# Kernel tuning notes

Measured on AMD Instinct MI355X. Metric: run time of the kernel, lower is better.

The kernel has to match this reference:

```python
import jax, jax.numpy as jnp
import numpy as np

# DeepseekV2MOE config (DeepSeek-V2-Lite-like, scaled)
T, H, E, I, K = 1024, 1024, 64, 512, 6
G, TKG = 8, 3          # n_group, topk_group
N_SHARED = 2
C = 256
SCALE = 2.5            # routed_scaling_factor


def setup_inputs() -> dict:
    key = jax.random.key(0)
    ks = jax.random.split(key, 7)
    inv = lambda d: 1.0 / np.sqrt(d).astype(np.float32)
    return {
        "hidden_states": jax.random.normal(ks[0], (T, H), jnp.float32),
        "gate_w": jax.random.normal(ks[1], (H, E), jnp.float32) * inv(H),
        "e_bias": jax.random.normal(ks[2], (E,), jnp.float32) * 0.01,  # e_score_correction_bias (noaux_tc)
        "w_gate_up": jax.random.normal(ks[3], (E, H, 2 * I), jnp.float32) * inv(H),
        "w_down": jax.random.normal(ks[4], (E, I, H), jnp.float32) * inv(I),
        "ws_gate_up": jax.random.normal(ks[5], (H, 2 * I * N_SHARED), jnp.float32) * inv(H),
        "ws_down": jax.random.normal(ks[6], (I * N_SHARED, H), jnp.float32) * inv(I * N_SHARED),
    }


def _silu_and_mul(gu):
    g, u = jnp.split(gu, 2, axis=-1)
    return jax.nn.silu(g) * u


def _grouped_topk(logits, bias):
    # DeepSeek-V3 noaux_tc grouped top-k with sigmoid scoring.
    scores = jax.nn.sigmoid(logits)                              # [T,E] original scores
    s = scores + bias[None, :]                                   # bias-corrected scores for selection
    grp = s.reshape(-1, G, E // G)
    grp_score = jax.lax.top_k(grp, 2)[0].sum(-1)                 # [T,G] sum of top-2 per group
    gidx = jax.lax.top_k(grp_score, TKG)[1]                      # [T,TKG]
    t = jnp.arange(s.shape[0])[:, None]
    gmask = jnp.zeros_like(grp_score, dtype=bool).at[t, gidx].set(True)
    emask = jnp.repeat(gmask, E // G, axis=1)                    # [T,E]
    eidx = jax.lax.top_k(jnp.where(emask, s, -jnp.inf), K)[1]    # [T,K]
    w = jnp.take_along_axis(scores, eidx, axis=1)                # weights from original (un-biased) scores
    w = w / w.sum(-1, keepdims=True)                             # renormalize (norm_topk_prob)
    return w, eidx


def _fused_moe(x, w, eidx, w_gate_up, w_down):
    # capacity-based dispatch -> grouped GEMM -> gather/scale combine
    A = x.shape[0] * K
    ef = eidx.reshape(A)                                         # expert id per assignment
    oh = jax.nn.one_hot(ef, E, dtype=jnp.int32)                  # [A,E]
    pos = ((jnp.cumsum(oh, axis=0) - 1) * oh).sum(-1)            # slot of each assignment within its expert
    xr = jnp.repeat(x, K, axis=0)                                # [A,H]
    xe = jnp.zeros((E, C, x.shape[1]), x.dtype).at[ef, pos].set(xr, mode="drop")  # [E,C,H]
    act = _silu_and_mul(jnp.einsum("ech,ehf->ecf", xe, w_gate_up))                # [E,C,I]
    ye = jnp.einsum("eci,eih->ech", act, w_down)                                   # [E,C,H]
    keep = (pos < C).astype(x.dtype)[:, None]
    yf = ye[ef, jnp.minimum(pos, C - 1)] * keep                  # [A,H]
    return (yf.reshape(-1, K, x.shape[1]) * w[..., None]).sum(1)  # [T,H]


def reference(hidden_states, gate_w, e_bias, w_gate_up, w_down, ws_gate_up, ws_down):
    shared = _silu_and_mul(hidden_states @ ws_gate_up) @ ws_down   # shared experts MLP
    logits = hidden_states @ gate_w                                # router
    w, eidx = _grouped_topk(logits, e_bias)
    routed = _fused_moe(hidden_states, w, eidx, w_gate_up, w_down)
    return routed * SCALE + shared                                 # non-fp16 branch
```

## Files before the change

### kernel.cpp

```cpp
#include <hip/hip_runtime.h>
#include <math.h>

typedef __bf16 bf16;
typedef bf16 bf16x8 __attribute__((ext_vector_type(8)));
typedef float f32x4 __attribute__((ext_vector_type(4)));
typedef unsigned int u32;

#define T_DIM 1024
#define H_DIM 1024
#define E_NUM 64
#define I_DIM 512
#define KTOP 6
#define TKG 3
#define CAP 256
#define A_TOT (T_DIM * KTOP)
#define SCALE_F 2.5f

#define BMx 128
#define BNx 128
#define BKx 64

typedef const u32 __attribute__((address_space(1)))* gas_t;
typedef u32 __attribute__((address_space(3)))* las_t;
__device__ __forceinline__ void gld16(const void* g, void* l) {
  __builtin_amdgcn_global_load_lds((gas_t)(unsigned long long)g,
                                   (las_t)(u32)(unsigned long long)l, 16, 0, 0);
}

__global__ __launch_bounds__(256) void cvt_bf16(const float* __restrict__ in,
                                                bf16* __restrict__ out) {
  int i = (blockIdx.x * 256 + threadIdx.x) * 4;
  float4 v = *(const float4*)(in + i);
  bf16 __align__(8) t[4] = {(bf16)v.x, (bf16)v.y, (bf16)v.z, (bf16)v.w};
  *(uint2*)(out + i) = *(const uint2*)t;
}

__global__ __launch_bounds__(256) void transpose_cvt(const float* __restrict__ in,
                                                     bf16* __restrict__ out,
                                                     int R, int C) {
  __shared__ bf16 tile[64][68];
  const long bb = (long)blockIdx.z * R * C;
  in += bb;
  out += bb;
  const int r0 = blockIdx.x * 64, c0 = blockIdx.y * 64;
  const int tid = threadIdx.x;
  const int lr = tid >> 4;
  const int lc = (tid & 15) * 4;
  #pragma unroll
  for (int rr = 0; rr < 64; rr += 16) {
    float4 v = *(const float4*)(in + (long)(r0 + lr + rr) * C + c0 + lc);
    bf16 __align__(8) t4[4] = {(bf16)v.x, (bf16)v.y, (bf16)v.z, (bf16)v.w};
    *(uint2*)(&tile[lr + rr][lc]) = *(const uint2*)t4;
  }
  __syncthreads();
  const int orow = tid >> 3;
  const int oc = (tid & 7) * 8;
  #pragma unroll
  for (int p = 0; p < 64; p += 32) {
    bf16 __align__(16) t8[8];
    #pragma unroll
    for (int j = 0; j < 8; ++j) t8[j] = tile[oc + j][orow + p];
    *(uint4*)(out + (long)(c0 + orow + p) * R + r0 + oc) = *(const uint4*)t8;
  }
}

__global__ __launch_bounds__(256) void router_topk(const float* __restrict__ x,
                                                   const float* __restrict__ gw,
                                                   const float* __restrict__ bias,
                                                   int* __restrict__ topk_id,
                                                   float* __restrict__ topk_w) {
  __shared__ float part[4][64];
  const int t = blockIdx.x;
  const int tid = threadIdx.x;
  const int wave = tid >> 6, lane = tid & 63;
  const float* xr = x + (long)t * H_DIM + wave * 256;
  float acc = 0.f;
  for (int h = 0; h < 256; h += 4) {
    float4 xv = *(const float4*)(xr + h);
    int hh = wave * 256 + h;
    acc += xv.x * gw[(hh + 0) * E_NUM + lane];
    acc += xv.y * gw[(hh + 1) * E_NUM + lane];
    acc += xv.z * gw[(hh + 2) * E_NUM + lane];
    acc += xv.w * gw[(hh + 3) * E_NUM + lane];
  }
  part[wave][lane] = acc;
  __syncthreads();
  if (wave != 0) return;
  acc = part[0][lane] + part[1][lane] + part[2][lane] + part[3][lane];

  float score = 1.f / (1.f + __expf(-acc));
  float sel = score + bias[lane];

  float m1 = sel, m2 = -INFINITY;
  #pragma unroll
  for (int off = 1; off < 8; off <<= 1) {
    float o1 = __shfl_xor(m1, off);
    float o2 = __shfl_xor(m2, off);
    float mn = fminf(m1, o1);
    float alt = (m1 >= o1) ? m2 : o2;
    m1 = fmaxf(m1, o1);
    m2 = fmaxf(mn, alt);
  }
  float gscore = m1 + m2;

  const int my_g = lane >> 3;
  unsigned gmask = 0;
  float gv = ((lane & 7) == 0) ? gscore : -INFINITY;
  for (int r = 0; r < TKG; ++r) {
    float v = gv;
    int idx = my_g;
    #pragma unroll
    for (int off = 1; off < 64; off <<= 1) {
      float ov = __shfl_xor(v, off);
      int oi = __shfl_xor(idx, off);
      if (ov > v || (ov == v && oi < idx)) { v = ov; idx = oi; }
    }
    gmask |= 1u << idx;
    if (my_g == idx) gv = -INFINITY;
  }

  float cand = ((gmask >> my_g) & 1u) ? sel : -INFINITY;
  float wk[KTOP];
  int ik[KTOP];
  float wsum = 0.f;
  for (int r = 0; r < KTOP; ++r) {
    float v = cand;
    int idx = lane;
    #pragma unroll
    for (int off = 1; off < 64; off <<= 1) {
      float ov = __shfl_xor(v, off);
      int oi = __shfl_xor(idx, off);
      if (ov > v || (ov == v && oi < idx)) { v = ov; idx = oi; }
    }
    float w = __shfl(score, idx);
    wk[r] = w; ik[r] = idx; wsum += w;
    if (lane == idx) cand = -INFINITY;
  }
  if (lane == 0) {
    float inv = 1.f / wsum;
    #pragma unroll
    for (int r = 0; r < KTOP; ++r) {
      topk_id[t * KTOP + r] = ik[r];
      topk_w[t * KTOP + r] = wk[r] * inv;
    }
  }
}

__global__ __launch_bounds__(64) void dispatch(const int* __restrict__ topk_id,
                                               int* __restrict__ rowlist,
                                               int* __restrict__ slot_a,
                                               int* __restrict__ counts) {
  __shared__ int ids[A_TOT];
  const int e = blockIdx.x, lane = threadIdx.x;
  for (int i = lane; i < A_TOT; i += 64) ids[i] = topk_id[i];
  __syncthreads();
  int base = 0;
  for (int a0 = 0; a0 < A_TOT; a0 += 64) {
    int a = a0 + lane;
    bool m = (ids[a] == e);
    unsigned long long bal = __ballot(m);
    if (m) {
      int pos = base + __popcll(bal & ((1ull << lane) - 1ull));
      slot_a[a] = (pos < CAP) ? pos : -1;
      if (pos < CAP) rowlist[e * CAP + pos] = a;
    }
    base += __popcll(bal);
  }
  if (lane == 0) counts[e] = (base < CAP) ? base : CAP;
}


__global__ __launch_bounds__(256) void gemm_gu(
    const bf16* __restrict__ X, int x_ld,
    const int* __restrict__ rows, const int* __restrict__ counts, int n_rows_fixed,
    const bf16* __restrict__ BT, long b_estride, int u_off,
    bf16* __restrict__ act, int act_ld, long act_estride, int kdim) {
  __shared__ union {
    struct { bf16 A[BMx * BKx]; bf16 B[BNx * BKx]; } st;
    bf16 epi[BMx * 72];
  } sm;
  const int e = blockIdx.z;
  const int n_rows = counts ? counts[e] : n_rows_fixed;
  const int m0 = blockIdx.x * BMx;
  if (m0 >= n_rows) return;
  const int nb = blockIdx.y;
  const int tid = threadIdx.x;
  const int w = tid >> 6, lane = tid & 63;
  const int q = lane >> 4, l16 = lane & 15;
  const int m_off = (w & 1) * 64;

  const int srow = w * 32 + (lane >> 3);
  const int gchunk = (lane & 7) ^ (lane >> 3);
  const bf16* pA[4];
  const bf16* pB[4];
  #pragma unroll
  for (int j = 0; j < 4; ++j) {
    int tr = m0 + srow + j * 8;
    int grow;
    if (rows) grow = (tr < n_rows) ? (rows[e * CAP + tr] / KTOP) : 0;
    else grow = tr;
    pA[j] = X + (long)grow * x_ld + gchunk * 8;
    int rB = srow + j * 8;
    int ng = (rB < 64) ? (nb * 64 + rB) : (u_off + nb * 64 + (rB - 64));
    pB[j] = BT + (long)e * b_estride + (long)ng * kdim + gchunk * 8;
  }
  bf16* ldsA = sm.st.A + w * 2048 + lane * 8;
  bf16* ldsB = sm.st.B + w * 2048 + lane * 8;

  f32x4 acc[4][4];
  #pragma unroll
  for (int i = 0; i < 4; ++i)
    #pragma unroll
    for (int j = 0; j < 4; ++j) acc[i][j] = (f32x4){0.f, 0.f, 0.f, 0.f};

  for (int k0 = 0; k0 < kdim; k0 += BKx) {
    #pragma unroll
    for (int j = 0; j < 4; ++j) {
      gld16(pA[j], ldsA + j * 512);
      gld16(pB[j], ldsB + j * 512);
      pA[j] += BKx;
      pB[j] += BKx;
    }
    __syncthreads();
    #pragma unroll
    for (int kh = 0; kh < 2; ++kh) {
      const int co = ((kh * 4 + q) ^ (l16 & 7)) * 8;
      bf16x8 a[4], b[4];
      #pragma unroll
      for (int i = 0; i < 4; ++i)
        a[i] = *(const bf16x8*)(sm.st.A + (m_off + i * 16 + l16) * BKx + co);
      #pragma unroll
      for (int j = 0; j < 4; ++j) {
        int nf = (j >> 1) * 64 + (w >> 1) * 32 + (j & 1) * 16;
        b[j] = *(const bf16x8*)(sm.st.B + (nf + l16) * BKx + co);
      }
      #pragma unroll
      for (int i = 0; i < 4; ++i)
        #pragma unroll
        for (int j = 0; j < 4; ++j)
          acc[i][j] = __builtin_amdgcn_mfma_f32_16x16x32_bf16(a[i], b[j], acc[i][j], 0, 0, 0);
    }
    __syncthreads();
  }

  const int c_base = (w >> 1) * 32;
  #pragma unroll
  for (int i = 0; i < 4; ++i)
    #pragma unroll
    for (int j = 0; j < 2; ++j)
      #pragma unroll
      for (int r = 0; r < 4; ++r) {
        float g = acc[i][j][r], uu = acc[i][j + 2][r];
        float s = g / (1.f + __expf(-g));
        sm.epi[(m_off + i * 16 + q * 4 + r) * 72 + c_base + j * 16 + l16] = (bf16)(s * uu);
      }
  __syncthreads();
  #pragma unroll
  for (int p = 0; p < 4; ++p) {
    int row = p * 32 + (tid >> 3);
    int c0 = (tid & 7) * 8;
    uint4 v = *(const uint4*)(sm.epi + row * 72 + c0);
    *(uint4*)(act + (long)e * act_estride + (long)(m0 + row) * act_ld + nb * 64 + c0) = v;
  }
}

template <typename OutT>
__global__ __launch_bounds__(256) void gemm_dn(
    const bf16* __restrict__ Abase, long a_estride, int a_ld,
    const int* __restrict__ rowsO, const int* __restrict__ counts, int n_rows_fixed,
    const bf16* __restrict__ BT, long b_estride,
    OutT* __restrict__ Out, int out_ld, int kdim) {
  __shared__ union {
    struct { bf16 A[BMx * BKx]; bf16 B[BNx * BKx]; } st;
    bf16 epi[BMx * 136];
  } sm;
  const int e = blockIdx.z;
  const int n_rows = counts ? counts[e] : n_rows_fixed;
  const int m0 = blockIdx.x * BMx;
  if (m0 >= n_rows) return;
  const int nb = blockIdx.y;
  const int tid = threadIdx.x;
  const int w = tid >> 6, lane = tid & 63;
  const int q = lane >> 4, l16 = lane & 15;
  const int m_off = (w & 1) * 64;
  const int n_off = (w >> 1) * 64;

  const int srow = w * 32 + (lane >> 3);
  const int gchunk = (lane & 7) ^ (lane >> 3);
  const bf16* pA[4];
  const bf16* pB[4];
  #pragma unroll
  for (int j = 0; j < 4; ++j) {
    pA[j] = Abase + (long)e * a_estride + (long)(m0 + srow + j * 8) * a_ld + gchunk * 8;
    pB[j] = BT + (long)e * b_estride + (long)(nb * BNx + srow + j * 8) * kdim + gchunk * 8;
  }
  bf16* ldsA = sm.st.A + w * 2048 + lane * 8;
  bf16* ldsB = sm.st.B + w * 2048 + lane * 8;

  f32x4 acc[4][4];
  #pragma unroll
  for (int i = 0; i < 4; ++i)
    #pragma unroll
    for (int j = 0; j < 4; ++j) acc[i][j] = (f32x4){0.f, 0.f, 0.f, 0.f};

  for (int k0 = 0; k0 < kdim; k0 += BKx) {
    #pragma unroll
    for (int j = 0; j < 4; ++j) {
      gld16(pA[j], ldsA + j * 512);
      gld16(pB[j], ldsB + j * 512);
      pA[j] += BKx;
      pB[j] += BKx;
    }
    __syncthreads();
    #pragma unroll
    for (int kh = 0; kh < 2; ++kh) {
      const int co = ((kh * 4 + q) ^ (l16 & 7)) * 8;
      bf16x8 a[4], b[4];
      #pragma unroll
      for (int i = 0; i < 4; ++i)
        a[i] = *(const bf16x8*)(sm.st.A + (m_off + i * 16 + l16) * BKx + co);
      #pragma unroll
      for (int j = 0; j < 4; ++j)
        b[j] = *(const bf16x8*)(sm.st.B + (n_off + j * 16 + l16) * BKx + co);
      #pragma unroll
      for (int i = 0; i < 4; ++i)
        #pragma unroll
        for (int j = 0; j < 4; ++j)
          acc[i][j] = __builtin_amdgcn_mfma_f32_16x16x32_bf16(a[i], b[j], acc[i][j], 0, 0, 0);
    }
    __syncthreads();
  }

  if constexpr (sizeof(OutT) == 4) {
    #pragma unroll
    for (int i = 0; i < 4; ++i)
      #pragma unroll
      for (int j = 0; j < 4; ++j)
        #pragma unroll
        for (int r = 0; r < 4; ++r) {
          int row = m0 + m_off + i * 16 + q * 4 + r;
          Out[(long)row * out_ld + nb * BNx + n_off + j * 16 + l16] = acc[i][j][r];
        }
  } else {
    #pragma unroll
    for (int i = 0; i < 4; ++i)
      #pragma unroll
      for (int j = 0; j < 4; ++j)
        #pragma unroll
        for (int r = 0; r < 4; ++r)
          sm.epi[(m_off + i * 16 + q * 4 + r) * 136 + n_off + j * 16 + l16] = (bf16)acc[i][j][r];
    __syncthreads();
    #pragma unroll
    for (int p = 0; p < 8; ++p) {
      int row = p * 16 + (tid >> 4);
      int c0 = (tid & 15) * 8;
      if (m0 + row < n_rows) {
        long orow = rowsO ? (long)rowsO[e * CAP + m0 + row] : (long)(m0 + row);
        *(uint4*)((bf16*)Out + orow * out_ld + nb * BNx + c0) =
            *(const uint4*)(sm.epi + row * 136 + c0);
      }
    }
  }
}

__global__ __launch_bounds__(256) void combine(const float* __restrict__ tkw,
                                               const int* __restrict__ slot_a,
                                               const bf16* __restrict__ Ya,
                                               float* __restrict__ out) {
  const int t = blockIdx.x, tid = threadIdx.x;
  long o = (long)t * H_DIM + tid * 4;
  float4 v = *(float4*)(out + o);
  float a0 = v.x, a1 = v.y, a2 = v.z, a3 = v.w;
  #pragma unroll
  for (int k = 0; k < KTOP; ++k) {
    int a = t * KTOP + k;
    if (slot_a[a] >= 0) {
      float w = tkw[a] * SCALE_F;
      const bf16* yr = Ya + (long)a * H_DIM + tid * 4;
      uint2 yv = *(const uint2*)yr;
      bf16 __align__(8) yb[4];
      *(uint2*)yb = yv;
      a0 += w * (float)yb[0];
      a1 += w * (float)yb[1];
      a2 += w * (float)yb[2];
      a3 += w * (float)yb[3];
    }
  }
  *(float4*)(out + o) = make_float4(a0, a1, a2, a3);
}

extern "C" void kernel_launch(void* const* d_in, const int* in_sizes, int n_in,
                              void* d_out, int out_size, void* d_ws, size_t ws_size,
                              hipStream_t stream) {
  const float* x     = (const float*)d_in[0];
  const float* gw    = (const float*)d_in[1];
  const float* bias  = (const float*)d_in[2];
  const float* w_gu  = (const float*)d_in[3];
  const float* w_dn  = (const float*)d_in[4];
  const float* ws_gu = (const float*)d_in[5];
  const float* ws_dn = (const float*)d_in[6];
  float* out = (float*)d_out;
  char* ws = (char*)d_ws;

  bf16* xbf     = (bf16*)(ws + 0);
  bf16* acts    = (bf16*)(ws + 2097152);
  bf16* actr    = (bf16*)(ws + 4194304);
  bf16* Ya      = (bf16*)(ws + 20971520);
  int*  tki     = (int*)(ws + 33554432);
  float* tkw    = (float*)(ws + 33579008);
  int*  rowlist = (int*)(ws + 33603584);
  int*  slot_a  = (int*)(ws + 33669120);
  int*  counts  = (int*)(ws + 33693696);
  bf16* wsguT   = (bf16*)(ws + 33694720);
  bf16* wsdnT   = (bf16*)(ws + 37889024);
  bf16* wguT    = (bf16*)(ws + 39986176);
  bf16* wdnT    = (bf16*)(ws + 39986176);

  cvt_bf16<<<dim3((T_DIM * H_DIM) / 1024), dim3(256), 0, stream>>>(x, xbf);
  router_topk<<<dim3(T_DIM), dim3(256), 0, stream>>>(x, gw, bias, tki, tkw);
  dispatch<<<dim3(E_NUM), dim3(64), 0, stream>>>(tki, rowlist, slot_a, counts);

  transpose_cvt<<<dim3(16, 16, 64), dim3(256), 0, stream>>>(w_gu, wguT, H_DIM, 2 * I_DIM);
  transpose_cvt<<<dim3(16, 32, 1), dim3(256), 0, stream>>>(ws_gu, wsguT, H_DIM, 2048);
  transpose_cvt<<<dim3(16, 16, 1), dim3(256), 0, stream>>>(ws_dn, wsdnT, 1024, H_DIM);

  gemm_gu<<<dim3(CAP / BMx, I_DIM / 64, E_NUM), dim3(256), 0, stream>>>(
      xbf, H_DIM, rowlist, counts, 0,
      wguT, (long)(2 * I_DIM) * H_DIM, I_DIM,
      actr, I_DIM, (long)CAP * I_DIM, H_DIM);

  gemm_gu<<<dim3(T_DIM / BMx, 1024 / 64, 1), dim3(256), 0, stream>>>(
      xbf, H_DIM, nullptr, nullptr, T_DIM,
      wsguT, 0, 1024,
      acts, 1024, 0, H_DIM);

  transpose_cvt<<<dim3(8, 16, 64), dim3(256), 0, stream>>>(w_dn, wdnT, I_DIM, H_DIM);

  gemm_dn<bf16><<<dim3(CAP / BMx, H_DIM / BNx, E_NUM), dim3(256), 0, stream>>>(
      actr, (long)CAP * I_DIM, I_DIM, rowlist, counts, 0,
      wdnT, (long)H_DIM * I_DIM,
      (bf16*)Ya, H_DIM, I_DIM);

  gemm_dn<float><<<dim3(T_DIM / BMx, H_DIM / BNx, 1), dim3(256), 0, stream>>>(
      acts, 0, 1024, nullptr, nullptr, T_DIM,
      wsdnT, 0,
      out, H_DIM, 1024);

  combine<<<dim3(T_DIM), dim3(256), 0, stream>>>(tkw, slot_a, Ya, out);
}
```

Baseline: 662.0 us.

## Fuse fp32 weight transpose and bf16 conversion into GEMM B-tile loads

Removes the separate transpose_cvt passes over all expert and shared weights. The GEMM kernels now read fp32 weights directly in their original layout, convert them to bf16 in registers, and write transposed, swizzled tiles into LDS, with the next k-tile's loads prefetched into registers. This avoids writing a full bf16 copy of the weights and reading it back. In exchange it adds register pressure, conversion ALU work in the main loop, and makes the B loads synchronous register loads instead of direct-to-LDS loads.

New measurement: 595.9 us. -10.0%, faster.

```diff
diff --git a/kernel.cpp b/kernel.cpp
--- a/kernel.cpp
+++ b/kernel.cpp
@@ -27,41 +27,16 @@
                                    (las_t)(u32)(unsigned long long)l, 16, 0, 0);
 }
 
+__device__ __forceinline__ int bswz(int n) {
+  return ((n >> 2) ^ ((n & 3) << 1)) & 7;
+}
+
 __global__ __launch_bounds__(256) void cvt_bf16(const float* __restrict__ in,
                                                 bf16* __restrict__ out) {
   int i = (blockIdx.x * 256 + threadIdx.x) * 4;
   float4 v = *(const float4*)(in + i);
   bf16 __align__(8) t[4] = {(bf16)v.x, (bf16)v.y, (bf16)v.z, (bf16)v.w};
   *(uint2*)(out + i) = *(const uint2*)t;
-}
-
-__global__ __launch_bounds__(256) void transpose_cvt(const float* __restrict__ in,
-                                                     bf16* __restrict__ out,
-                                                     int R, int C) {
-  __shared__ bf16 tile[64][68];
-  const long bb = (long)blockIdx.z * R * C;
-  in += bb;
-  out += bb;
-  const int r0 = blockIdx.x * 64, c0 = blockIdx.y * 64;
-  const int tid = threadIdx.x;
-  const int lr = tid >> 4;
-  const int lc = (tid & 15) * 4;
-  #pragma unroll
-  for (int rr = 0; rr < 64; rr += 16) {
-    float4 v = *(const float4*)(in + (long)(r0 + lr + rr) * C + c0 + lc);
-    bf16 __align__(8) t4[4] = {(bf16)v.x, (bf16)v.y, (bf16)v.z, (bf16)v.w};
-    *(uint2*)(&tile[lr + rr][lc]) = *(const uint2*)t4;
-  }
-  __syncthreads();
-  const int orow = tid >> 3;
-  const int oc = (tid & 7) * 8;
-  #pragma unroll
-  for (int p = 0; p < 64; p += 32) {
-    bf16 __align__(16) t8[8];
-    #pragma unroll
-    for (int j = 0; j < 8; ++j) t8[j] = tile[oc + j][orow + p];
-    *(uint4*)(out + (long)(c0 + orow + p) * R + r0 + oc) = *(const uint4*)t8;
-  }
 }
 
 __global__ __launch_bounds__(256) void router_topk(const float* __restrict__ x,
@@ -173,7 +148,7 @@
 __global__ __launch_bounds__(256) void gemm_gu(
     const bf16* __restrict__ X, int x_ld,
     const int* __restrict__ rows, const int* __restrict__ counts, int n_rows_fixed,
-    const bf16* __restrict__ BT, long b_estride, int u_off,
+    const float* __restrict__ W, long w_estride, int ldb, int u_off,
     bf16* __restrict__ act, int act_ld, long act_estride, int kdim) {
   __shared__ union {
     struct { bf16 A[BMx * BKx]; bf16 B[BNx * BKx]; } st;
@@ -192,7 +167,6 @@
   const int srow = w * 32 + (lane >> 3);
   const int gchunk = (lane & 7) ^ (lane >> 3);
   const bf16* pA[4];
-  const bf16* pB[4];
   #pragma unroll
   for (int j = 0; j < 4; ++j) {
     int tr = m0 + srow + j * 8;
@@ -200,12 +174,16 @@
     if (rows) grow = (tr < n_rows) ? (rows[e * CAP + tr] / KTOP) : 0;
     else grow = tr;
     pA[j] = X + (long)grow * x_ld + gchunk * 8;
-    int rB = srow + j * 8;
-    int ng = (rB < 64) ? (nb * 64 + rB) : (u_off + nb * 64 + (rB - 64));
-    pB[j] = BT + (long)e * b_estride + (long)ng * kdim + gchunk * 8;
   }
   bf16* ldsA = sm.st.A + w * 2048 + lane * 8;
-  bf16* ldsB = sm.st.B + w * 2048 + lane * 8;
+
+  const int kc = tid >> 5;
+  const int n0 = (tid & 31) * 4;
+  const int gcol = (n0 < 64) ? (nb * 64 + n0) : (u_off + nb * 64 + (n0 - 64));
+  const float* bcol = W + (long)e * w_estride + (long)kc * 8 * ldb + gcol;
+  float4 bv[8];
+  #pragma unroll
+  for (int r = 0; r < 8; ++r) bv[r] = *(const float4*)(bcol + (long)r * ldb);
 
   f32x4 acc[4][4];
   #pragma unroll
@@ -217,22 +195,34 @@
     #pragma unroll
     for (int j = 0; j < 4; ++j) {
       gld16(pA[j], ldsA + j * 512);
-      gld16(pB[j], ldsB + j * 512);
       pA[j] += BKx;
-      pB[j] += BKx;
+    }
+    #pragma unroll
+    for (int j = 0; j < 4; ++j) {
+      bf16 __align__(16) t8[8];
+      #pragma unroll
+      for (int r = 0; r < 8; ++r) t8[r] = (bf16)((const float*)&bv[r])[j];
+      int n = n0 + j;
+      *(uint4*)(sm.st.B + n * BKx + ((kc ^ bswz(n)) * 8)) = *(const uint4*)t8;
+    }
+    if (k0 + BKx < kdim) {
+      const float* bnext = bcol + (long)(k0 + BKx) * ldb;
+      #pragma unroll
+      for (int r = 0; r < 8; ++r) bv[r] = *(const float4*)(bnext + (long)r * ldb);
     }
     __syncthreads();
     #pragma unroll
     for (int kh = 0; kh < 2; ++kh) {
+      bf16x8 a[4], b[4];
       const int co = ((kh * 4 + q) ^ (l16 & 7)) * 8;
-      bf16x8 a[4], b[4];
       #pragma unroll
       for (int i = 0; i < 4; ++i)
         a[i] = *(const bf16x8*)(sm.st.A + (m_off + i * 16 + l16) * BKx + co);
       #pragma unroll
       for (int j = 0; j < 4; ++j) {
         int nf = (j >> 1) * 64 + (w >> 1) * 32 + (j & 1) * 16;
-        b[j] = *(const bf16x8*)(sm.st.B + (nf + l16) * BKx + co);
+        int n = nf + l16;
+        b[j] = *(const bf16x8*)(sm.st.B + n * BKx + (((kh * 4 + q) ^ bswz(n)) * 8));
       }
       #pragma unroll
       for (int i = 0; i < 4; ++i)
@@ -268,7 +258,7 @@
 __global__ __launch_bounds__(256) void gemm_dn(
     const bf16* __restrict__ Abase, long a_estride, int a_ld,
     const int* __restrict__ rowsO, const int* __restrict__ counts, int n_rows_fixed,
-    const bf16* __restrict__ BT, long b_estride,
+    const float* __restrict__ W, long w_estride, int ldb,
     OutT* __restrict__ Out, int out_ld, int kdim) {
   __shared__ union {
     struct { bf16 A[BMx * BKx]; bf16 B[BNx * BKx]; } st;
@@ -288,14 +278,17 @@
   const int srow = w * 32 + (lane >> 3);
   const int gchunk = (lane & 7) ^ (lane >> 3);
   const bf16* pA[4];
-  const bf16* pB[4];
-  #pragma unroll
-  for (int j = 0; j < 4; ++j) {
+  #pragma unroll
+  for (int j = 0; j < 4; ++j)
     pA[j] = Abase + (long)e * a_estride + (long)(m0 + srow + j * 8) * a_ld + gchunk * 8;
-    pB[j] = BT + (long)e * b_estride + (long)(nb * BNx + srow + j * 8) * kdim + gchunk * 8;
-  }
   bf16* ldsA = sm.st.A + w * 2048 + lane * 8;
-  bf16* ldsB = sm.st.B + w * 2048 + lane * 8;
+
+  const int kc = tid >> 5;
+  const int n0 = (tid & 31) * 4;
+  const float* bcol = W + (long)e * w_estride + (long)kc * 8 * ldb + nb * BNx + n0;
+  float4 bv[8];
+  #pragma unroll
+  for (int r = 0; r < 8; ++r) bv[r] = *(const float4*)(bcol + (long)r * ldb);
 
   f32x4 acc[4][4];
   #pragma unroll
@@ -307,21 +300,34 @@
     #pragma unroll
     for (int j = 0; j < 4; ++j) {
       gld16(pA[j], ldsA + j * 512);
-      gld16(pB[j], ldsB + j * 512);
       pA[j] += BKx;
-      pB[j] += BKx;
+    }
+    #pragma unroll
+    for (int j = 0; j < 4; ++j) {
+      bf16 __align__(16) t8[8];
+      #pragma unroll
+      for (int r = 0; r < 8; ++r) t8[r] = (bf16)((const float*)&bv[r])[j];
+      int n = n0 + j;
+      *(uint4*)(sm.st.B + n * BKx + ((kc ^ bswz(n)) * 8)) = *(const uint4*)t8;
+    }
+    if (k0 + BKx < kdim) {
+      const float* bnext = bcol + (long)(k0 + BKx) * ldb;
+      #pragma unroll
+      for (int r = 0; r < 8; ++r) bv[r] = *(const float4*)(bnext + (long)r * ldb);
     }
     __syncthreads();
     #pragma unroll
     for (int kh = 0; kh < 2; ++kh) {
+      bf16x8 a[4], b[4];
       const int co = ((kh * 4 + q) ^ (l16 & 7)) * 8;
-      bf16x8 a[4], b[4];
       #pragma unroll
       for (int i = 0; i < 4; ++i)
         a[i] = *(const bf16x8*)(sm.st.A + (m_off + i * 16 + l16) * BKx + co);
       #pragma unroll
-      for (int j = 0; j < 4; ++j)
-        b[j] = *(const bf16x8*)(sm.st.B + (n_off + j * 16 + l16) * BKx + co);
+      for (int j = 0; j < 4; ++j) {
+        int n = n_off + j * 16 + l16;
+        b[j] = *(const bf16x8*)(sm.st.B + n * BKx + (((kh * 4 + q) ^ bswz(n)) * 8));
+      }
       #pragma unroll
       for (int i = 0; i < 4; ++i)
         #pragma unroll
@@ -411,39 +417,29 @@
   int*  rowlist = (int*)(ws + 33603584);
   int*  slot_a  = (int*)(ws + 33669120);
   int*  counts  = (int*)(ws + 33693696);
-  bf16* wsguT   = (bf16*)(ws + 33694720);
-  bf16* wsdnT   = (bf16*)(ws + 37889024);
-  bf16* wguT    = (bf16*)(ws + 39986176);
-  bf16* wdnT    = (bf16*)(ws + 39986176);
 
   cvt_bf16<<<dim3((T_DIM * H_DIM) / 1024), dim3(256), 0, stream>>>(x, xbf);
   router_topk<<<dim3(T_DIM), dim3(256), 0, stream>>>(x, gw, bias, tki, tkw);
   dispatch<<<dim3(E_NUM), dim3(64), 0, stream>>>(tki, rowlist, slot_a, counts);
 
-  transpose_cvt<<<dim3(16, 16, 64), dim3(256), 0, stream>>>(w_gu, wguT, H_DIM, 2 * I_DIM);
-  transpose_cvt<<<dim3(16, 32, 1), dim3(256), 0, stream>>>(ws_gu, wsguT, H_DIM, 2048);
-  transpose_cvt<<<dim3(16, 16, 1), dim3(256), 0, stream>>>(ws_dn, wsdnT, 1024, H_DIM);
-
   gemm_gu<<<dim3(CAP / BMx, I_DIM / 64, E_NUM), dim3(256), 0, stream>>>(
       xbf, H_DIM, rowlist, counts, 0,
-      wguT, (long)(2 * I_DIM) * H_DIM, I_DIM,
+      w_gu, (long)H_DIM * 2 * I_DIM, 2 * I_DIM, I_DIM,
       actr, I_DIM, (long)CAP * I_DIM, H_DIM);
 
   gemm_gu<<<dim3(T_DIM / BMx, 1024 / 64, 1), dim3(256), 0, stream>>>(
       xbf, H_DIM, nullptr, nullptr, T_DIM,
-      wsguT, 0, 1024,
+      ws_gu, 0, 2048, 1024,
       acts, 1024, 0, H_DIM);
-
-  transpose_cvt<<<dim3(8, 16, 64), dim3(256), 0, stream>>>(w_dn, wdnT, I_DIM, H_DIM);
 
   gemm_dn<bf16><<<dim3(CAP / BMx, H_DIM / BNx, E_NUM), dim3(256), 0, stream>>>(
       actr, (long)CAP * I_DIM, I_DIM, rowlist, counts, 0,
-      wdnT, (long)H_DIM * I_DIM,
+      w_dn, (long)I_DIM * H_DIM, H_DIM,
       (bf16*)Ya, H_DIM, I_DIM);
 
   gemm_dn<float><<<dim3(T_DIM / BMx, H_DIM / BNx, 1), dim3(256), 0, stream>>>(
       acts, 0, 1024, nullptr, nullptr, T_DIM,
-      wsdnT, 0,
+      ws_dn, 0, H_DIM,
       out, H_DIM, 1024);
 
   combine<<<dim3(T_DIM), dim3(256), 0, stream>>>(tkw, slot_a, Ya, out);
```
